# Performance work log

Measured on AMD Instinct MI355X. Metric: run time of the kernel, lower is better.

Reference implementation:

```python
import jax, jax.numpy as jnp
import numpy as np

DIM = 512
HEADS = 8
DIM_HEAD = 64
INNER = HEADS * DIM_HEAD
SCALE = DIM_HEAD ** -0.5


def setup_inputs() -> dict:
    key = jax.random.key(0)
    ks = jax.random.split(key, 6)
    x = jax.random.normal(ks[0], (8, 1024, DIM), dtype=jnp.float32)
    # nn.Linear(dim, inner, bias=False): y = x @ W.T ; store W as [out, in]
    wq = jax.random.normal(ks[1], (INNER, DIM), dtype=jnp.float32) * (DIM ** -0.5)
    wk = jax.random.normal(ks[2], (INNER, DIM), dtype=jnp.float32) * (DIM ** -0.5)
    wv = jax.random.normal(ks[3], (INNER, DIM), dtype=jnp.float32) * (DIM ** -0.5)
    wo = jax.random.normal(ks[4], (DIM, INNER), dtype=jnp.float32) * (INNER ** -0.5)
    bo = jax.random.normal(ks[5], (DIM,), dtype=jnp.float32) * 0.01
    return {"x": x, "wq": wq, "wk": wk, "wv": wv, "wo": wo, "bo": bo}


def reference(x, wq, wk, wv, wo, bo):
    b, n, _ = x.shape
    # QKV projections -> [b, h, n, d]
    def proj(w):
        return (x @ w.T).reshape(b, n, HEADS, DIM_HEAD).transpose(0, 2, 1, 3)
    q, k, v = proj(wq), proj(wk), proj(wv)
    dots = jnp.einsum('bhid,bhjd->bhij', q, k) * SCALE
    dots = jnp.clip(dots, 1e-6, 1.0)
    dots_exp = jnp.exp(dots)
    attn = dots_exp / jnp.sum(dots_exp, axis=-1, keepdims=True)
    out = jnp.einsum('bhij,bhjd->bhid', attn, v)  # [b,h,n,d]
    out = out.transpose(0, 2, 1, 3).reshape(b, n, INNER)
    return out @ wo.T + bo
```

## Files before the change

### kernel.cpp

```cpp
#include <hip/hip_runtime.h>
#include <hip/hip_fp16.h>

#define BATCH 8
#define SEQ   1024
#define DIM   512
#define HEADS 8
#define DHEAD 64
#define MTOT  (BATCH*SEQ)

typedef _Float16 f16x8 __attribute__((ext_vector_type(8)));
typedef _Float16 f16x4 __attribute__((ext_vector_type(4)));
typedef float    fx4   __attribute__((ext_vector_type(4)));

#define MFMA16 __builtin_amdgcn_mfma_f32_16x16x32_f16

__global__ __launch_bounds__(256) void convert_k(
    const float* __restrict__ x,  const float* __restrict__ wq,
    const float* __restrict__ wk, const float* __restrict__ wv,
    const float* __restrict__ wo,
    _Float16* __restrict__ xb, _Float16* __restrict__ wqkvb,
    _Float16* __restrict__ wob)
{
    const int XU = (MTOT*DIM)/4;
    const int WU = (DIM*DIM)/4;
    int idx = blockIdx.x*256 + threadIdx.x;
    if (idx >= XU + 4*WU) return;
    const float* src; _Float16* dst;
    if (idx < XU) { src = x + idx*4; dst = xb + idx*4; }
    else {
        int t = idx - XU; int region = t >> 16; int off = (t & 65535)*4;
        if      (region == 0) { src = wq + off; dst = wqkvb + off; }
        else if (region == 1) { src = wk + off; dst = wqkvb + DIM*DIM + off; }
        else if (region == 2) { src = wv + off; dst = wqkvb + 2*DIM*DIM + off; }
        else                  { src = wo + off; dst = wob + off; }
    }
    float4 v = *(const float4*)src;
    f16x4 o = { (_Float16)v.x, (_Float16)v.y, (_Float16)v.z, (_Float16)v.w };
    *(f16x4*)dst = o;
}

__global__ __launch_bounds__(256,2) void qkv_proj(
    const _Float16* __restrict__ A, const _Float16* __restrict__ B,
    _Float16* __restrict__ Qb, _Float16* __restrict__ Kb,
    _Float16* __restrict__ VTb)
{
    __shared__ _Float16 lA[128*72];
    __shared__ _Float16 lB[128*72];
    const int tid = threadIdx.x;
    const int m0 = blockIdx.y*128, n0 = blockIdx.x*128;
    const int w = tid>>6, l = tid&63, lr = l&15, lq = l>>4;
    const int wr = w>>1, wc = w&1;
    fx4 acc[4][4] = {};

    for (int k0 = 0; k0 < DIM; k0 += 64) {
        __syncthreads();
#pragma unroll
        for (int i = 0; i < 4; i++) {
            int u = tid + i*256;
            int row = u >> 3, cu = (u & 7)*8;
            *(f16x8*)&lA[row*72 + cu] = *(const f16x8*)&A[(m0+row)*DIM + k0 + cu];
            *(f16x8*)&lB[row*72 + cu] = *(const f16x8*)&B[(n0+row)*DIM + k0 + cu];
        }
        __syncthreads();
#pragma unroll
        for (int kb = 0; kb < 2; kb++) {
            f16x8 af[4], bf[4];
#pragma unroll
            for (int cb = 0; cb < 4; cb++)
                bf[cb] = *(const f16x8*)&lB[(wc*64+cb*16+lr)*72 + kb*32 + lq*8];
#pragma unroll
            for (int rb = 0; rb < 4; rb++)
                af[rb] = *(const f16x8*)&lA[(wr*64+rb*16+lr)*72 + kb*32 + lq*8];
#pragma unroll
            for (int rb = 0; rb < 4; rb++)
#pragma unroll
                for (int cb = 0; cb < 4; cb++)
                    acc[rb][cb] = MFMA16(af[rb], bf[cb], acc[rb][cb], 0,0,0);
        }
    }
    if (n0 >= 1024) {
#pragma unroll
        for (int rb = 0; rb < 4; rb++)
#pragma unroll
            for (int cb = 0; cb < 4; cb++) {
                int inner = (n0 - 1024) + wc*64 + cb*16 + lr;
                int h = inner >> 6, d = inner & 63;
                int m = m0 + wr*64 + rb*16 + lq*4;
                int b = m >> 10, n = m & 1023;
                f16x4 v4;
#pragma unroll
                for (int i = 0; i < 4; i++) v4[i] = (_Float16)acc[rb][cb][i];
                *(f16x4*)&VTb[((size_t)(b*HEADS+h)*DHEAD + d)*SEQ + n] = v4;
            }
    } else {
#pragma unroll
        for (int rb = 0; rb < 4; rb++)
#pragma unroll
            for (int cb = 0; cb < 4; cb++) {
                int nn = n0 + wc*64 + cb*16 + lr;
                int which = nn >> 9, inner = nn & 511, h = inner >> 6, d = inner & 63;
#pragma unroll
                for (int i = 0; i < 4; i++) {
                    int m = m0 + wr*64 + rb*16 + lq*4 + i;
                    int b = m >> 10, n = m & 1023;
                    float v = acc[rb][cb][i];
                    if (which == 0)
                        Qb[((b*HEADS+h)*SEQ + n)*DHEAD + d] = (_Float16)(v * 0.125f);
                    else
                        Kb[((b*HEADS+h)*SEQ + n)*DHEAD + d] = (_Float16)v;
                }
            }
    }
}

__global__ __launch_bounds__(512,4) void attn_k(
    const _Float16* __restrict__ Q, const _Float16* __restrict__ K,
    const _Float16* __restrict__ VT, _Float16* __restrict__ AO)
{
    __shared__ _Float16 lKV[128*72];
    __shared__ _Float16 lP[8][16*136];
    const int tid = threadIdx.x;
    const int w = tid>>6, l = tid&63, lr = l&15, lq = l>>4;
    const int bh = blockIdx.y, q0 = blockIdx.x*128;
    const int b = bh>>3, h = bh&7;
    const _Float16* Qp = Q  + (size_t)bh*SEQ*DHEAD;
    const _Float16* Kp = K  + (size_t)bh*SEQ*DHEAD;
    const _Float16* Vp = VT + (size_t)bh*DHEAD*SEQ;

    f16x8 qf[2];
#pragma unroll
    for (int kb = 0; kb < 2; kb++)
        qf[kb] = *(const f16x8*)&Qp[(q0 + w*16 + lr)*DHEAD + kb*32 + lq*8];

    fx4 O[4] = {};
    fx4 lsum = {};

    for (int kt = 0; kt < 8; kt++) {
        int k0 = kt*128;
        __syncthreads();
#pragma unroll
        for (int i = 0; i < 2; i++) {
            int u = tid + i*512;
            int row = u >> 3, cu = (u & 7)*8;
            *(f16x8*)&lKV[row*72 + cu] = *(const f16x8*)&Kp[(k0+row)*DHEAD + cu];
        }
        __syncthreads();
#pragma unroll
        for (int cb = 0; cb < 8; cb++) {
            f16x8 kf[2];
#pragma unroll
            for (int kb = 0; kb < 2; kb++)
                kf[kb] = *(const f16x8*)&lKV[(cb*16+lr)*72 + kb*32 + lq*8];
            fx4 s = {};
            s = MFMA16(qf[0], kf[0], s, 0,0,0);
            s = MFMA16(qf[1], kf[1], s, 0,0,0);
            int pbase = (lq*4)*136 + (((cb*2 + (lr>>3)) ^ (lq<<1))*8) + (lr&7);
#pragma unroll
            for (int i = 0; i < 4; i++) {
                float p = __expf(__builtin_amdgcn_fmed3f(s[i], 1e-6f, 1.0f));
                lsum[i] += p;
                lP[w][pbase + i*136] = (_Float16)p;
            }
        }
        __syncthreads();
#pragma unroll
        for (int i = 0; i < 2; i++) {
            int u = tid + i*512;
            int row = u >> 4, cu = (u & 15)*8;
            *(f16x8*)&lKV[row*136 + cu] = *(const f16x8*)&Vp[row*SEQ + k0 + cu];
        }
        __syncthreads();
#pragma unroll
        for (int ks = 0; ks < 4; ks++) {
            f16x8 af = *(const f16x8*)
                &lP[w][lr*136 + (((ks*4 + lq) ^ (((lr>>2)&3)<<1))*8)];
#pragma unroll
            for (int db = 0; db < 4; db++) {
                f16x8 vf = *(const f16x8*)&lKV[(db*16+lr)*136 + ks*32 + lq*8];
                O[db] = MFMA16(af, vf, O[db], 0,0,0);
            }
        }
    }
#pragma unroll
    for (int i = 0; i < 4; i++) {
        float s = lsum[i];
        s += __shfl_xor(s, 1);
        s += __shfl_xor(s, 2);
        s += __shfl_xor(s, 4);
        s += __shfl_xor(s, 8);
        lsum[i] = s;
    }
    fx4 inv;
#pragma unroll
    for (int i = 0; i < 4; i++) inv[i] = 1.0f / lsum[i];
#pragma unroll
    for (int db = 0; db < 4; db++)
#pragma unroll
        for (int i = 0; i < 4; i++) {
            int n = q0 + w*16 + lq*4 + i;
            int d = db*16 + lr;
            AO[((size_t)(b*SEQ + n)*HEADS + h)*DHEAD + d] =
                (_Float16)(O[db][i] * inv[i]);
        }
}

__global__ __launch_bounds__(256,2) void out_proj(
    const _Float16* __restrict__ A, const _Float16* __restrict__ B,
    const float* __restrict__ bo, float* __restrict__ out)
{
    __shared__ _Float16 lA[128*72];
    __shared__ _Float16 lB[128*72];
    const int tid = threadIdx.x;
    const int m0 = blockIdx.y*128, n0 = blockIdx.x*128;
    const int w = tid>>6, l = tid&63, lr = l&15, lq = l>>4;
    const int wr = w>>1, wc = w&1;
    fx4 acc[4][4] = {};

    for (int k0 = 0; k0 < DIM; k0 += 64) {
        __syncthreads();
#pragma unroll
        for (int i = 0; i < 4; i++) {
            int u = tid + i*256;
            int row = u >> 3, cu = (u & 7)*8;
            *(f16x8*)&lA[row*72 + cu] = *(const f16x8*)&A[(m0+row)*DIM + k0 + cu];
            *(f16x8*)&lB[row*72 + cu] = *(const f16x8*)&B[(n0+row)*DIM + k0 + cu];
        }
        __syncthreads();
#pragma unroll
        for (int kb = 0; kb < 2; kb++) {
            f16x8 af[4], bf[4];
#pragma unroll
            for (int cb = 0; cb < 4; cb++)
                bf[cb] = *(const f16x8*)&lB[(wc*64+cb*16+lr)*72 + kb*32 + lq*8];
#pragma unroll
            for (int rb = 0; rb < 4; rb++)
                af[rb] = *(const f16x8*)&lA[(wr*64+rb*16+lr)*72 + kb*32 + lq*8];
#pragma unroll
            for (int rb = 0; rb < 4; rb++)
#pragma unroll
                for (int cb = 0; cb < 4; cb++)
                    acc[rb][cb] = MFMA16(af[rb], bf[cb], acc[rb][cb], 0,0,0);
        }
    }
#pragma unroll
    for (int rb = 0; rb < 4; rb++)
#pragma unroll
        for (int cb = 0; cb < 4; cb++) {
            int nn = n0 + wc*64 + cb*16 + lr;
            float bias = bo[nn];
#pragma unroll
            for (int i = 0; i < 4; i++) {
                int m = m0 + wr*64 + rb*16 + lq*4 + i;
                out[(size_t)m*DIM + nn] = acc[rb][cb][i] + bias;
            }
        }
}

extern "C" void kernel_launch(void* const* d_in, const int* in_sizes, int n_in,
                              void* d_out, int out_size, void* d_ws, size_t ws_size,
                              hipStream_t stream)
{
    const float* x  = (const float*)d_in[0];
    const float* wq = (const float*)d_in[1];
    const float* wk = (const float*)d_in[2];
    const float* wv = (const float*)d_in[3];
    const float* wo = (const float*)d_in[4];
    const float* bo = (const float*)d_in[5];
    float* out = (float*)d_out;
    char* ws = (char*)d_ws;

    _Float16* xb    = (_Float16*)(ws);
    _Float16* wqkvb = (_Float16*)(ws + 8388608);
    _Float16* wob   = (_Float16*)(ws + 9961472);
    _Float16* Qb    = (_Float16*)(ws + 10485760);
    _Float16* Kb    = (_Float16*)(ws + 18874368);
    _Float16* VTb   = (_Float16*)(ws + 27262976);
    _Float16* attnb = (_Float16*)(ws);

    convert_k<<<5120, 256, 0, stream>>>(x, wq, wk, wv, wo, xb, wqkvb, wob);
    qkv_proj<<<dim3(12, 64), 256, 0, stream>>>(xb, wqkvb, Qb, Kb, VTb);
    attn_k<<<dim3(8, 64), 512, 0, stream>>>(Qb, Kb, VTb, attnb);
    out_proj<<<dim3(4, 64), 256, 0, stream>>>(attnb, wob, bo, out);
}
```

Measured before the change: 168.9 us.

## Use direct global-to-LDS loads and restructure attention to transposed S with fewer syncs

```diff
diff --git a/kernel.cpp b/kernel.cpp
--- a/kernel.cpp
+++ b/kernel.cpp
@@ -13,6 +13,12 @@
 typedef float    fx4   __attribute__((ext_vector_type(4)));
 
 #define MFMA16 __builtin_amdgcn_mfma_f32_16x16x32_f16
+
+__device__ __forceinline__ void gload16(const _Float16* g, _Float16* l) {
+    __builtin_amdgcn_global_load_lds(
+        (const __attribute__((address_space(1))) unsigned int*)g,
+        (__attribute__((address_space(3))) unsigned int*)l, 16, 0, 0);
+}
 
 __global__ __launch_bounds__(256) void convert_k(
     const float* __restrict__ x,  const float* __restrict__ wq,
@@ -39,27 +45,27 @@
     *(f16x4*)dst = o;
 }
 
-__global__ __launch_bounds__(256,2) void qkv_proj(
+__global__ __launch_bounds__(256,3) void qkv_proj(
     const _Float16* __restrict__ A, const _Float16* __restrict__ B,
     _Float16* __restrict__ Qb, _Float16* __restrict__ Kb,
     _Float16* __restrict__ VTb)
 {
-    __shared__ _Float16 lA[128*72];
-    __shared__ _Float16 lB[128*72];
+    __shared__ _Float16 lA[128*64];
+    __shared__ _Float16 lB[128*64];
     const int tid = threadIdx.x;
     const int m0 = blockIdx.y*128, n0 = blockIdx.x*128;
     const int w = tid>>6, l = tid&63, lr = l&15, lq = l>>4;
     const int wr = w>>1, wc = w&1;
+    const int srow = (l>>3), scol = (l&7)*8;
     fx4 acc[4][4] = {};
 
     for (int k0 = 0; k0 < DIM; k0 += 64) {
         __syncthreads();
 #pragma unroll
-        for (int i = 0; i < 4; i++) {
-            int u = tid + i*256;
-            int row = u >> 3, cu = (u & 7)*8;
-            *(f16x8*)&lA[row*72 + cu] = *(const f16x8*)&A[(m0+row)*DIM + k0 + cu];
-            *(f16x8*)&lB[row*72 + cu] = *(const f16x8*)&B[(n0+row)*DIM + k0 + cu];
+        for (int t = 0; t < 4; t++) {
+            int row = w*32 + t*8;
+            gload16(&A[(size_t)(m0+row+srow)*DIM + k0 + scol], &lA[row*64]);
+            gload16(&B[(size_t)(n0+row+srow)*DIM + k0 + scol], &lB[row*64]);
         }
         __syncthreads();
 #pragma unroll
@@ -67,10 +73,10 @@
             f16x8 af[4], bf[4];
 #pragma unroll
             for (int cb = 0; cb < 4; cb++)
-                bf[cb] = *(const f16x8*)&lB[(wc*64+cb*16+lr)*72 + kb*32 + lq*8];
-#pragma unroll
-            for (int rb = 0; rb < 4; rb++)
-                af[rb] = *(const f16x8*)&lA[(wr*64+rb*16+lr)*72 + kb*32 + lq*8];
+                bf[cb] = *(const f16x8*)&lB[(wc*64+cb*16+lr)*64 + kb*32 + lq*8];
+#pragma unroll
+            for (int rb = 0; rb < 4; rb++)
+                af[rb] = *(const f16x8*)&lA[(wr*64+rb*16+lr)*64 + kb*32 + lq*8];
 #pragma unroll
             for (int rb = 0; rb < 4; rb++)
 #pragma unroll
@@ -113,19 +119,21 @@
     }
 }
 
-__global__ __launch_bounds__(512,4) void attn_k(
+__global__ __launch_bounds__(256,4) void attn_k(
     const _Float16* __restrict__ Q, const _Float16* __restrict__ K,
     const _Float16* __restrict__ VT, _Float16* __restrict__ AO)
 {
-    __shared__ _Float16 lKV[128*72];
-    __shared__ _Float16 lP[8][16*136];
+    __shared__ _Float16 lK[128*64];
+    __shared__ _Float16 lVT[64*136];
+    __shared__ _Float16 lPT[4][16*48];
     const int tid = threadIdx.x;
     const int w = tid>>6, l = tid&63, lr = l&15, lq = l>>4;
-    const int bh = blockIdx.y, q0 = blockIdx.x*128;
+    const int bh = blockIdx.y, q0 = blockIdx.x*64;
     const int b = bh>>3, h = bh&7;
     const _Float16* Qp = Q  + (size_t)bh*SEQ*DHEAD;
     const _Float16* Kp = K  + (size_t)bh*SEQ*DHEAD;
     const _Float16* Vp = VT + (size_t)bh*DHEAD*SEQ;
+    const int srow = (l>>3), scol = (l&7)*8;
 
     f16x8 qf[2];
 #pragma unroll
@@ -133,97 +141,86 @@
         qf[kb] = *(const f16x8*)&Qp[(q0 + w*16 + lr)*DHEAD + kb*32 + lq*8];
 
     fx4 O[4] = {};
-    fx4 lsum = {};
+    float lsum = 0.0f;
 
     for (int kt = 0; kt < 8; kt++) {
         int k0 = kt*128;
         __syncthreads();
 #pragma unroll
-        for (int i = 0; i < 2; i++) {
-            int u = tid + i*512;
-            int row = u >> 3, cu = (u & 7)*8;
-            *(f16x8*)&lKV[row*72 + cu] = *(const f16x8*)&Kp[(k0+row)*DHEAD + cu];
-        }
-        __syncthreads();
-#pragma unroll
-        for (int cb = 0; cb < 8; cb++) {
-            f16x8 kf[2];
-#pragma unroll
-            for (int kb = 0; kb < 2; kb++)
-                kf[kb] = *(const f16x8*)&lKV[(cb*16+lr)*72 + kb*32 + lq*8];
-            fx4 s = {};
-            s = MFMA16(qf[0], kf[0], s, 0,0,0);
-            s = MFMA16(qf[1], kf[1], s, 0,0,0);
-            int pbase = (lq*4)*136 + (((cb*2 + (lr>>3)) ^ (lq<<1))*8) + (lr&7);
-#pragma unroll
-            for (int i = 0; i < 4; i++) {
-                float p = __expf(__builtin_amdgcn_fmed3f(s[i], 1e-6f, 1.0f));
-                lsum[i] += p;
-                lP[w][pbase + i*136] = (_Float16)p;
-            }
-        }
-        __syncthreads();
-#pragma unroll
-        for (int i = 0; i < 2; i++) {
-            int u = tid + i*512;
+        for (int t = 0; t < 4; t++) {
+            int row = w*32 + t*8;
+            gload16(&Kp[(size_t)(k0+row+srow)*DHEAD + scol], &lK[row*64]);
+        }
+#pragma unroll
+        for (int i = 0; i < 4; i++) {
+            int u = tid + i*256;
             int row = u >> 4, cu = (u & 15)*8;
-            *(f16x8*)&lKV[row*136 + cu] = *(const f16x8*)&Vp[row*SEQ + k0 + cu];
-        }
-        __syncthreads();
+            *(f16x8*)&lVT[row*136 + cu] = *(const f16x8*)&Vp[(size_t)row*SEQ + k0 + cu];
+        }
+        __syncthreads();
+
 #pragma unroll
         for (int ks = 0; ks < 4; ks++) {
-            f16x8 af = *(const f16x8*)
-                &lP[w][lr*136 + (((ks*4 + lq) ^ (((lr>>2)&3)<<1))*8)];
+#pragma unroll
+            for (int half = 0; half < 2; half++) {
+                int rb = ks*2 + half;
+                f16x8 kf0 = *(const f16x8*)&lK[(rb*16+lr)*64 + lq*8];
+                f16x8 kf1 = *(const f16x8*)&lK[(rb*16+lr)*64 + 32 + lq*8];
+                fx4 s = {};
+                s = MFMA16(kf0, qf[0], s, 0,0,0);
+                s = MFMA16(kf1, qf[1], s, 0,0,0);
+                f16x4 p4;
+#pragma unroll
+                for (int i = 0; i < 4; i++) {
+                    float p = __expf(__builtin_amdgcn_fmed3f(s[i], 1e-6f, 1.0f));
+                    lsum += p;
+                    p4[i] = (_Float16)p;
+                }
+                *(f16x4*)&lPT[w][lr*48 + half*16 + lq*4] = p4;
+            }
+            f16x8 pf = *(const f16x8*)&lPT[w][lr*48 + lq*8];
 #pragma unroll
             for (int db = 0; db < 4; db++) {
-                f16x8 vf = *(const f16x8*)&lKV[(db*16+lr)*136 + ks*32 + lq*8];
-                O[db] = MFMA16(af, vf, O[db], 0,0,0);
-            }
-        }
-    }
-#pragma unroll
-    for (int i = 0; i < 4; i++) {
-        float s = lsum[i];
-        s += __shfl_xor(s, 1);
-        s += __shfl_xor(s, 2);
-        s += __shfl_xor(s, 4);
-        s += __shfl_xor(s, 8);
-        lsum[i] = s;
-    }
-    fx4 inv;
-#pragma unroll
-    for (int i = 0; i < 4; i++) inv[i] = 1.0f / lsum[i];
-#pragma unroll
-    for (int db = 0; db < 4; db++)
-#pragma unroll
-        for (int i = 0; i < 4; i++) {
-            int n = q0 + w*16 + lq*4 + i;
-            int d = db*16 + lr;
-            AO[((size_t)(b*SEQ + n)*HEADS + h)*DHEAD + d] =
-                (_Float16)(O[db][i] * inv[i]);
-        }
-}
-
-__global__ __launch_bounds__(256,2) void out_proj(
+                f16x8 vf = *(const f16x8*)&lVT[(db*16+lr)*136 + ks*32 + lq*8];
+                O[db] = MFMA16(vf, pf, O[db], 0,0,0);
+            }
+        }
+    }
+    lsum += __shfl_xor(lsum, 16);
+    lsum += __shfl_xor(lsum, 32);
+    float inv = 1.0f / lsum;
+
+    const int n = q0 + w*16 + lr;
+    _Float16* aop = AO + ((size_t)(b*SEQ + n)*HEADS + h)*DHEAD;
+#pragma unroll
+    for (int db = 0; db < 4; db++) {
+        f16x4 o4;
+#pragma unroll
+        for (int i = 0; i < 4; i++) o4[i] = (_Float16)(O[db][i] * inv);
+        *(f16x4*)&aop[db*16 + lq*4] = o4;
+    }
+}
+
+__global__ __launch_bounds__(256,3) void out_proj(
     const _Float16* __restrict__ A, const _Float16* __restrict__ B,
     const float* __restrict__ bo, float* __restrict__ out)
 {
-    __shared__ _Float16 lA[128*72];
-    __shared__ _Float16 lB[128*72];
+    __shared__ _Float16 lA[128*64];
+    __shared__ _Float16 lB[128*64];
     const int tid = threadIdx.x;
     const int m0 = blockIdx.y*128, n0 = blockIdx.x*128;
     const int w = tid>>6, l = tid&63, lr = l&15, lq = l>>4;
     const int wr = w>>1, wc = w&1;
+    const int srow = (l>>3), scol = (l&7)*8;
     fx4 acc[4][4] = {};
 
     for (int k0 = 0; k0 < DIM; k0 += 64) {
         __syncthreads();
 #pragma unroll
-        for (int i = 0; i < 4; i++) {
-            int u = tid + i*256;
-            int row = u >> 3, cu = (u & 7)*8;
-            *(f16x8*)&lA[row*72 + cu] = *(const f16x8*)&A[(m0+row)*DIM + k0 + cu];
-            *(f16x8*)&lB[row*72 + cu] = *(const f16x8*)&B[(n0+row)*DIM + k0 + cu];
+        for (int t = 0; t < 4; t++) {
+            int row = w*32 + t*8;
+            gload16(&A[(size_t)(m0+row+srow)*DIM + k0 + scol], &lA[row*64]);
+            gload16(&B[(size_t)(n0+row+srow)*DIM + k0 + scol], &lB[row*64]);
         }
         __syncthreads();
 #pragma unroll
@@ -231,10 +228,10 @@
             f16x8 af[4], bf[4];
 #pragma unroll
             for (int cb = 0; cb < 4; cb++)
-                bf[cb] = *(const f16x8*)&lB[(wc*64+cb*16+lr)*72 + kb*32 + lq*8];
-#pragma unroll
-            for (int rb = 0; rb < 4; rb++)
-                af[rb] = *(const f16x8*)&lA[(wr*64+rb*16+lr)*72 + kb*32 + lq*8];
+                bf[cb] = *(const f16x8*)&lB[(wc*64+cb*16+lr)*64 + kb*32 + lq*8];
+#pragma unroll
+            for (int rb = 0; rb < 4; rb++)
+                af[rb] = *(const f16x8*)&lA[(wr*64+rb*16+lr)*64 + kb*32 + lq*8];
 #pragma unroll
             for (int rb = 0; rb < 4; rb++)
 #pragma unroll
@@ -279,6 +276,6 @@
 
     convert_k<<<5120, 256, 0, stream>>>(x, wq, wk, wv, wo, xb, wqkvb, wob);
     qkv_proj<<<dim3(12, 64), 256, 0, stream>>>(xb, wqkvb, Qb, Kb, VTb);
-    attn_k<<<dim3(8, 64), 512, 0, stream>>>(Qb, Kb, VTb, attnb);
+    attn_k<<<dim3(16, 64), 256, 0, stream>>>(Qb, Kb, VTb, attnb);
     out_proj<<<dim3(4, 64), 256, 0, stream>>>(attnb, wob, bo, out);
 }
```

After: 157.7 us. 1.07x faster.
